# Kernel optimization log

Measured on AMD Instinct MI355X. Metric: run time of the kernel, lower is better.

## Reference

```python
import jax, jax.numpy as jnp
import numpy as np

B, N, D, C = 256, 200000, 128, 1000


def _l2_normalize(v, axis=-1, eps=1e-12):
    # matches torch F.normalize(p=2): v / max(||v||, eps)
    norm = jnp.sqrt(jnp.sum(v * v, axis=axis, keepdims=True))
    return v / jnp.maximum(norm, eps)


def setup_inputs() -> dict:
    key = jax.random.key(0)
    k1, k2, k3 = jax.random.split(key, 3)
    x = jax.random.normal(k1, (B, D), dtype=jnp.float32)
    index_embeddings = jax.random.normal(k2, (N, D), dtype=jnp.float32)
    class_labels = jax.random.randint(k3, (N,), 0, C, dtype=jnp.int32)
    return {
        "x": x,
        "index_embeddings": index_embeddings,
        "class_labels": class_labels,
        "num_classes": C,
    }


def reference(x, index_embeddings, class_labels, num_classes):
    # backbone output flattened -> embeddings [B, D]; L2-normalize (queries and index,
    # index normalization happens in add_index_data in the original module)
    emb = _l2_normalize(x)
    idx_emb = _l2_normalize(index_embeddings)
    # cosine similarities [B, N]
    similarities = jnp.einsum('bd,nd->bn', emb, idx_emb)
    # per-class max reduction (replaces Python loop over classes):
    # segment-max over the index dimension keyed by class_labels -> [B, num_classes]
    logits = jax.ops.segment_max(
        similarities.T, class_labels, num_segments=num_classes,
        indices_are_sorted=False,
    ).T
    return logits
```

## Files before the change

### kernel.cpp

```cpp
#include <hip/hip_runtime.h>
#include <hip/hip_bf16.h>
#include <stdint.h>

#define D_ 128
#define NB 64
#define NINF (-__builtin_inff())

typedef float f32x4 __attribute__((ext_vector_type(4)));
typedef short bf16x8 __attribute__((ext_vector_type(8)));

__device__ inline unsigned short f2bf(float f){
  unsigned x = __float_as_uint(f);
  return (unsigned short)((x + 0x7FFFu + ((x >> 16) & 1u)) >> 16);
}
__device__ inline unsigned packbf(float a, float b){
  return (unsigned)f2bf(a) | ((unsigned)f2bf(b) << 16);
}
__device__ inline unsigned fkey(float v){
  unsigned b = __float_as_uint(v);
  return (b & 0x80000000u) ? ~b : (b | 0x80000000u);
}

__global__ void k_prep(const float* __restrict__ emb, const float* __restrict__ x,
                       unsigned short* __restrict__ nrmlin, unsigned short* __restrict__ xn,
                       const int* __restrict__ lab, unsigned* __restrict__ hist,
                       int N, int B, int C, int PN, int XB, int HB){
  const int bid = blockIdx.x;
  const int t = threadIdx.x;
  if (bid < PN + XB){
    const float* src; unsigned short* dst; int nrows; int r0;
    if (bid < PN){ src = emb; dst = nrmlin; nrows = N; r0 = bid * 64; }
    else         { src = x;   dst = xn;     nrows = B; r0 = (bid - PN) * 64; }
    int r = r0 + (t >> 2);
    if (r >= nrows) return;
    int j = t & 3;
    const f32x4* s4 = reinterpret_cast<const f32x4*>(src + (size_t)r * D_ + j * 32);
    f32x4 v[8];
    #pragma unroll
    for (int i = 0; i < 8; i++) v[i] = s4[i];
    float ss = 0.f;
    #pragma unroll
    for (int i = 0; i < 8; i++) ss += v[i][0]*v[i][0] + v[i][1]*v[i][1] + v[i][2]*v[i][2] + v[i][3]*v[i][3];
    ss += __shfl_xor(ss, 1); ss += __shfl_xor(ss, 2);
    float sc = 1.0f / fmaxf(sqrtf(ss), 1e-12f);
    unsigned o[16];
    #pragma unroll
    for (int i = 0; i < 8; i++){
      o[i*2]   = packbf(v[i][0]*sc, v[i][1]*sc);
      o[i*2+1] = packbf(v[i][2]*sc, v[i][3]*sc);
    }
    uint4* d4 = reinterpret_cast<uint4*>(dst + (size_t)r * D_ + j * 32);
    #pragma unroll
    for (int i = 0; i < 4; i++) d4[i] = make_uint4(o[i*4], o[i*4+1], o[i*4+2], o[i*4+3]);
  } else {
    int hb = bid - PN - XB;
    __shared__ unsigned lh[1024];
    for (int c = t; c < 1024; c += 256) lh[c] = 0;
    __syncthreads();
    for (int i = hb * 256 + t; i < N; i += HB * 256) atomicAdd(&lh[lab[i]], 1u);
    __syncthreads();
    for (int c = t; c < C; c += 256){ unsigned v = lh[c]; if (v) atomicAdd(&hist[c], v); }
  }
}

__global__ void k_scan(const unsigned* __restrict__ hist, unsigned* __restrict__ cursor,
                       unsigned* __restrict__ cbase, int C){
  __shared__ unsigned s[1024];
  int t = threadIdx.x;
  unsigned v = (t < C) ? hist[t] : 0u;
  s[t] = v; __syncthreads();
  for (int off = 1; off < 1024; off <<= 1){
    unsigned u = (t >= off) ? s[t - off] : 0u;
    __syncthreads();
    s[t] += u;
    __syncthreads();
  }
  if (t < C){ unsigned e = s[t] - v; cursor[t] = e; cbase[t] = e; }
}

__global__ void k_scatter(const int* __restrict__ lab, unsigned* __restrict__ cursor,
                          int* __restrict__ perm, int* __restrict__ slab, int N){
  for (int i = blockIdx.x * 256 + threadIdx.x; i < N; i += gridDim.x * 256){
    int c = lab[i];
    unsigned pos = atomicAdd(&cursor[c], 1u);
    perm[pos] = i;
    slab[pos] = c;
  }
}

__global__ __launch_bounds__(256, 2) void k_gemm_cls(
    const unsigned short* __restrict__ nrmlin,
    const unsigned short* __restrict__ xn,
    const int* __restrict__ perm,
    const unsigned* __restrict__ cbase, const unsigned* __restrict__ hist,
    float* __restrict__ out, int N, int C){
  const int c = blockIdx.x;
  const int t = threadIdx.x, w = t >> 6, lane = t & 63, lr = lane & 15, lg = lane >> 4;
  const int nrows = (int)hist[c];
  if (nrows == 0){ out[(size_t)t * C + c] = NINF; return; }
  const int base = (int)cbase[c];
  const int last = base + nrows - 1;
  const int chunks = (nrows + NB - 1) >> 6;

  __shared__ __align__(16) unsigned short Ab[2][NB * D_];

  auto rid_load = [&](int ci, int (&r)[4]){
    int cc = ci < chunks ? ci : chunks - 1;
    #pragma unroll
    for (int i = 0; i < 4; i++){
      int gr = base + cc * NB + i * 16 + lr;
      if (gr > last) gr = last;
      r[i] = perm[gr];
    }
  };
  auto stage = [&](int bb, const int (&r)[4]){
    #pragma unroll
    for (int i = 0; i < 4; i++){
      const char* src = (const char*)nrmlin + (size_t)r[i] * 256 + ((w * 4 + lg) << 4);
      char* dst = (char*)(&Ab[bb][0]) + (w + i * 4) * 1024 + lane * 16;
      __builtin_amdgcn_global_load_lds(
          (const __attribute__((address_space(1))) unsigned int*)src,
          (__attribute__((address_space(3))) unsigned int*)dst, 16, 0, 0);
    }
  };

  int ridN[4];
  rid_load(0, ridN);
  stage(0, ridN);
  rid_load(1, ridN);

  bf16x8 bf[4][4];
  #pragma unroll
  for (int ni = 0; ni < 4; ni++)
    #pragma unroll
    for (int kk = 0; kk < 4; kk++)
      bf[ni][kk] = *reinterpret_cast<const bf16x8*>(
          xn + (size_t)(w * 64 + ni * 16 + lr) * D_ + kk * 32 + lg * 8);

  float M0 = NINF, M1 = NINF, M2 = NINF, M3 = NINF;

  for (int ci = 0; ci < chunks; ++ci){
    const int b = ci & 1;
    stage(b ^ 1, ridN);
    rid_load(ci + 2, ridN);
    __builtin_amdgcn_s_barrier();

    f32x4 acc[4][4];
    #pragma unroll
    for (int mi = 0; mi < 4; mi++)
      #pragma unroll
      for (int ni = 0; ni < 4; ni++)
        acc[mi][ni] = (f32x4){0.f, 0.f, 0.f, 0.f};

    #pragma unroll
    for (int mi = 0; mi < 4; mi++)
      #pragma unroll
      for (int kk = 0; kk < 4; kk++){
        bf16x8 af = *reinterpret_cast<const bf16x8*>(&Ab[b][(mi * 4 + kk) * 512 + lane * 8]);
        #pragma unroll
        for (int ni = 0; ni < 4; ni++)
          acc[mi][ni] = __builtin_amdgcn_mfma_f32_16x16x32_bf16(af, bf[ni][kk], acc[mi][ni], 0, 0, 0);
      }
    __builtin_amdgcn_s_barrier();

    #pragma unroll
    for (int mi = 0; mi < 4; mi++)
      #pragma unroll
      for (int rg = 0; rg < 4; rg++){
        M0 = fmaxf(M0, acc[mi][0][rg]);
        M1 = fmaxf(M1, acc[mi][1][rg]);
        M2 = fmaxf(M2, acc[mi][2][rg]);
        M3 = fmaxf(M3, acc[mi][3][rg]);
      }
  }
  asm volatile("s_waitcnt vmcnt(0)" ::: "memory");

  M0 = fmaxf(M0, __shfl_xor(M0, 16)); M0 = fmaxf(M0, __shfl_xor(M0, 32));
  M1 = fmaxf(M1, __shfl_xor(M1, 16)); M1 = fmaxf(M1, __shfl_xor(M1, 32));
  M2 = fmaxf(M2, __shfl_xor(M2, 16)); M2 = fmaxf(M2, __shfl_xor(M2, 32));
  M3 = fmaxf(M3, __shfl_xor(M3, 16)); M3 = fmaxf(M3, __shfl_xor(M3, 32));
  float mv = (lg < 2) ? ((lg == 0) ? M0 : M1) : ((lg == 2) ? M2 : M3);
  out[(size_t)t * C + c] = mv;
}

__global__ void k_init_out(unsigned* __restrict__ o, int n){
  int i = blockIdx.x * 256 + threadIdx.x;
  if (i < n) o[i] = 0x007FFFFFu;
}

struct __align__(16) GSm {
  unsigned short A[NB * 136];
  float sims[16 * 257];
  float scale[NB];
  int rowid[NB];
  int clab[NB];
};

__global__ __launch_bounds__(256, 2) void k_gemm_gather(
    const float* __restrict__ emb, const unsigned short* __restrict__ xn,
    const int* __restrict__ perm, const int* __restrict__ slab,
    unsigned* __restrict__ out_u, int N, int C){
  __shared__ GSm sm;
  const int t = threadIdx.x;
  const int base = blockIdx.x * NB;
  if (t < NB){
    int p = base + t; if (p > N - 1) p = N - 1;
    sm.rowid[t] = perm[p];
    sm.clab[t]  = slab[p];
  }
  __syncthreads();
  {
    int r = t >> 2, j = t & 3;
    const float4* src = reinterpret_cast<const float4*>(emb + (long)sm.rowid[r] * D_ + j * 32);
    float4 v[8];
    #pragma unroll
    for (int i = 0; i < 8; i++) v[i] = src[i];
    float ss = 0.f;
    #pragma unroll
    for (int i = 0; i < 8; i++) ss += v[i].x*v[i].x + v[i].y*v[i].y + v[i].z*v[i].z + v[i].w*v[i].w;
    ss += __shfl_xor(ss, 1); ss += __shfl_xor(ss, 2);
    sm.scale[r] = 1.0f / fmaxf(sqrtf(ss), 1e-12f);
    unsigned* dst = reinterpret_cast<unsigned*>(&sm.A[r * 136 + j * 32]);
    #pragma unroll
    for (int i = 0; i < 8; i++){
      dst[i * 2]     = packbf(v[i].x, v[i].y);
      dst[i * 2 + 1] = packbf(v[i].z, v[i].w);
    }
  }
  const int w = t >> 6, lane = t & 63;
  const int lr = lane & 15, lg = lane >> 4;
  bf16x8 bfr[4][4];
  #pragma unroll
  for (int ni = 0; ni < 4; ni++)
    #pragma unroll
    for (int kk = 0; kk < 4; kk++)
      bfr[ni][kk] = *reinterpret_cast<const bf16x8*>(
          xn + (size_t)(w * 64 + ni * 16 + lr) * D_ + kk * 32 + lg * 8);
  f32x4 acc[4][4];
  #pragma unroll
  for (int mi = 0; mi < 4; mi++)
    #pragma unroll
    for (int ni = 0; ni < 4; ni++)
      acc[mi][ni] = (f32x4){0.f, 0.f, 0.f, 0.f};
  __syncthreads();
  #pragma unroll
  for (int mi = 0; mi < 4; mi++)
    #pragma unroll
    for (int kk = 0; kk < 4; kk++){
      bf16x8 af = *reinterpret_cast<const bf16x8*>(&sm.A[(mi * 16 + lr) * 136 + kk * 32 + lg * 8]);
      #pragma unroll
      for (int ni = 0; ni < 4; ni++)
        acc[mi][ni] = __builtin_amdgcn_mfma_f32_16x16x32_bf16(af, bfr[ni][kk], acc[mi][ni], 0, 0, 0);
    }
  int cur = -1; float rm = 0.f;
  for (int mi = 0; mi < 4; mi++){
    __syncthreads();
    #pragma unroll
    for (int ni = 0; ni < 4; ni++)
      #pragma unroll
      for (int rg = 0; rg < 4; rg++){
        int r16 = lg * 4 + rg;
        sm.sims[r16 * 257 + w * 64 + ni * 16 + lr] = acc[mi][ni][rg] * sm.scale[mi * 16 + r16];
      }
    __syncthreads();
    #pragma unroll
    for (int r16 = 0; r16 < 16; r16++){
      int cc = sm.clab[mi * 16 + r16];
      float v = sm.sims[r16 * 257 + t];
      if (cc != cur){
        if (cur >= 0) atomicMax(&out_u[(size_t)t * C + cur], fkey(rm));
        cur = cc; rm = v;
      } else rm = fmaxf(rm, v);
    }
  }
  atomicMax(&out_u[(size_t)t * C + cur], fkey(rm));
}

__global__ void k_finalize(unsigned* __restrict__ o, int n){
  int i = blockIdx.x * 256 + threadIdx.x;
  if (i < n){
    unsigned k = o[i];
    o[i] = (k & 0x80000000u) ? (k & 0x7FFFFFFFu) : ~k;
  }
}

extern "C" void kernel_launch(void* const* d_in, const int* in_sizes, int n_in,
                              void* d_out, int out_size, void* d_ws, size_t ws_size,
                              hipStream_t stream){
  const float* x   = (const float*)d_in[0];
  const float* emb = (const float*)d_in[1];
  const int*   lab = (const int*)d_in[2];
  const int B = in_sizes[0] / D_;
  const int N = in_sizes[1] / D_;
  const int C = out_size / B;

  const int PNfull = (N + 63) / 64;
  const int XB = (B + 63) / 64;
  const int HB = 208;

  char* ws = (char*)d_ws;
  size_t off = 0;
  unsigned short* xn = (unsigned short*)(ws); off += ((size_t)B * D_ * 2 + 255) & ~(size_t)255;
  unsigned* hist   = (unsigned*)(ws + off); off += 4096;
  unsigned* cursor = (unsigned*)(ws + off); off += 4096;
  unsigned* cbase  = (unsigned*)(ws + off); off += 4096;
  size_t narr = ((size_t)N * 4 + 255) & ~(size_t)255;
  int* perm   = (int*)(ws + off); off += narr;
  int* slab   = (int*)(ws + off); off += narr;
  unsigned short* nrmlin = (unsigned short*)(ws + off);
  size_t need = off + (size_t)N * D_ * 2;
  const bool fast = (ws_size >= need);
  const int PN = fast ? PNfull : 0;

  hipMemsetAsync(hist, 0, 4096, stream);
  k_prep<<<PN + XB + HB, 256, 0, stream>>>(emb, x, nrmlin, xn, lab, hist,
                                           N, B, C, PN, XB, HB);
  k_scan<<<1, 1024, 0, stream>>>(hist, cursor, cbase, C);
  k_scatter<<<208, 256, 0, stream>>>(lab, cursor, perm, slab, N);
  if (fast){
    k_gemm_cls<<<C, 256, 0, stream>>>(nrmlin, xn, perm, cbase, hist,
                                      (float*)d_out, N, C);
  } else {
    const int IB = (B * C + 255) / 256;
    k_init_out<<<IB, 256, 0, stream>>>((unsigned*)d_out, B * C);
    k_gemm_gather<<<PNfull, 256, 0, stream>>>(emb, xn, perm, slab, (unsigned*)d_out, N, C);
    k_finalize<<<IB, 256, 0, stream>>>((unsigned*)d_out, B * C);
  }
}
```

Before: 243.1 us.

## Fuse all stages into one cooperative persistent kernel with grid syncs

Replaces the memset, prep, scan, scatter and per-class GEMM launches with a single cooperative kernel of 512 blocks. Stages are separated by grid.sync, and per-block histograms are reduced through a phist buffer instead of global atomics. The intent is to remove launch gaps and inter-kernel idle time. The cost is several grid-wide barriers and a fixed grid size that handles 1000 classes in about two waves, which may imbalance the GEMM phase. It falls back to the old multi-kernel path if the cooperative launch fails or the workspace is too small.

```diff
diff --git a/kernel.cpp b/kernel.cpp
--- a/kernel.cpp
+++ b/kernel.cpp
@@ -1,9 +1,13 @@
 #include <hip/hip_runtime.h>
 #include <hip/hip_bf16.h>
+#include <hip/hip_cooperative_groups.h>
 #include <stdint.h>
+
+namespace cg = cooperative_groups;
 
 #define D_ 128
 #define NB 64
+#define GB 512
 #define NINF (-__builtin_inff())
 
 typedef float f32x4 __attribute__((ext_vector_type(4)));
@@ -19,6 +23,187 @@
 __device__ inline unsigned fkey(float v){
   unsigned b = __float_as_uint(v);
   return (b & 0x80000000u) ? ~b : (b | 0x80000000u);
+}
+
+__device__ inline void norm_unit(const float* __restrict__ src, unsigned short* __restrict__ dst,
+                                 int r0, int t){
+  int r = r0 + (t >> 2), j = t & 3;
+  const f32x4* s4 = reinterpret_cast<const f32x4*>(src + (size_t)r * D_ + j * 32);
+  f32x4 v[8];
+  #pragma unroll
+  for (int i = 0; i < 8; i++) v[i] = s4[i];
+  float ss = 0.f;
+  #pragma unroll
+  for (int i = 0; i < 8; i++) ss += v[i][0]*v[i][0] + v[i][1]*v[i][1] + v[i][2]*v[i][2] + v[i][3]*v[i][3];
+  ss += __shfl_xor(ss, 1); ss += __shfl_xor(ss, 2);
+  float sc = 1.0f / fmaxf(sqrtf(ss), 1e-12f);
+  unsigned o[16];
+  #pragma unroll
+  for (int i = 0; i < 8; i++){
+    o[i*2]   = packbf(v[i][0]*sc, v[i][1]*sc);
+    o[i*2+1] = packbf(v[i][2]*sc, v[i][3]*sc);
+  }
+  uint4* d4 = reinterpret_cast<uint4*>(dst + (size_t)r * D_ + j * 32);
+  #pragma unroll
+  for (int i = 0; i < 4; i++) d4[i] = make_uint4(o[i*4], o[i*4+1], o[i*4+2], o[i*4+3]);
+}
+
+__global__ __launch_bounds__(256, 2) void k_all(
+    const float* __restrict__ emb, const float* __restrict__ x,
+    const int* __restrict__ lab,
+    unsigned short* __restrict__ nrmlin, unsigned short* __restrict__ xn,
+    unsigned* __restrict__ phist, unsigned* __restrict__ hist,
+    unsigned* __restrict__ cursor, unsigned* __restrict__ cbase,
+    int* __restrict__ perm, float* __restrict__ out,
+    int N, int B, int C){
+  cg::grid_group grid = cg::this_grid();
+  const int bid = blockIdx.x, t = threadIdx.x;
+  const int nblk = (int)gridDim.x;
+  const int w = t >> 6, lane = t & 63, lr = lane & 15, lg = lane >> 4;
+
+  __shared__ __align__(16) unsigned short Ab[2][NB * D_];
+  unsigned* lh = reinterpret_cast<unsigned*>(&Ab[0][0]);
+
+  for (int c = t; c < 1024; c += 256) lh[c] = 0;
+  __syncthreads();
+  const int PN = N >> 6;
+  const int XU = B >> 6;
+  for (int u = bid; u < PN + XU; u += nblk){
+    if (u < PN) norm_unit(emb, nrmlin, u * 64, t);
+    else        norm_unit(x,   xn,    (u - PN) * 64, t);
+  }
+  for (int i = bid * 256 + t; i < N; i += nblk * 256) atomicAdd(&lh[lab[i]], 1u);
+  __syncthreads();
+  for (int c = t; c < C; c += 256) phist[(size_t)bid * 1024 + c] = lh[c];
+  __threadfence();
+  grid.sync();
+
+  {
+    int gw = (bid << 2) + w;
+    for (int c = gw; c < C; c += nblk * 4){
+      int s = 0;
+      for (int p = lane; p < nblk; p += 64) s += (int)phist[(size_t)p * 1024 + c];
+      #pragma unroll
+      for (int m = 32; m >= 1; m >>= 1) s += __shfl_xor(s, m);
+      if (lane == 0) hist[c] = (unsigned)s;
+    }
+  }
+  __threadfence();
+  grid.sync();
+
+  if (bid == 0){
+    unsigned v[4]; unsigned s = 0;
+    #pragma unroll
+    for (int i = 0; i < 4; i++){ int c = t * 4 + i; v[i] = (c < C) ? hist[c] : 0u; s += v[i]; }
+    lh[t] = s; __syncthreads();
+    for (int off = 1; off < 256; off <<= 1){
+      unsigned u2 = (t >= off) ? lh[t - off] : 0u;
+      __syncthreads(); lh[t] += u2; __syncthreads();
+    }
+    unsigned run = lh[t] - s;
+    #pragma unroll
+    for (int i = 0; i < 4; i++){
+      int c = t * 4 + i;
+      if (c < C){ cursor[c] = run; cbase[c] = run; }
+      run += v[i];
+    }
+  }
+  __threadfence();
+  grid.sync();
+
+  for (int i = bid * 256 + t; i < N; i += nblk * 256){
+    int c = lab[i];
+    unsigned pos = atomicAdd(&cursor[c], 1u);
+    perm[pos] = i;
+  }
+  __threadfence();
+  grid.sync();
+
+  bf16x8 bf[4][4];
+  #pragma unroll
+  for (int ni = 0; ni < 4; ni++)
+    #pragma unroll
+    for (int kk = 0; kk < 4; kk++)
+      bf[ni][kk] = *reinterpret_cast<const bf16x8*>(
+          xn + (size_t)(w * 64 + ni * 16 + lr) * D_ + kk * 32 + lg * 8);
+
+  for (int c = bid; c < C; c += nblk){
+    const int nrows = (int)hist[c];
+    if (nrows == 0){ out[(size_t)t * C + c] = NINF; continue; }
+    const int base = (int)cbase[c];
+    const int last = base + nrows - 1;
+    const int chunks = (nrows + NB - 1) >> 6;
+
+    auto rid_load = [&](int ci, int (&r)[4]){
+      int cc = ci < chunks ? ci : chunks - 1;
+      #pragma unroll
+      for (int i = 0; i < 4; i++){
+        int gr = base + cc * NB + i * 16 + lr;
+        if (gr > last) gr = last;
+        r[i] = perm[gr];
+      }
+    };
+    auto stage = [&](int bb, const int (&r)[4]){
+      #pragma unroll
+      for (int i = 0; i < 4; i++){
+        const char* src = (const char*)nrmlin + (size_t)r[i] * 256 + ((w * 4 + lg) << 4);
+        char* dst = (char*)(&Ab[bb][0]) + (w + i * 4) * 1024 + lane * 16;
+        __builtin_amdgcn_global_load_lds(
+            (const __attribute__((address_space(1))) unsigned int*)src,
+            (__attribute__((address_space(3))) unsigned int*)dst, 16, 0, 0);
+      }
+    };
+
+    int ridN[4];
+    rid_load(0, ridN);
+    stage(0, ridN);
+    rid_load(1, ridN);
+
+    float M0 = NINF, M1 = NINF, M2 = NINF, M3 = NINF;
+
+    for (int ci = 0; ci < chunks; ++ci){
+      const int b = ci & 1;
+      stage(b ^ 1, ridN);
+      rid_load(ci + 2, ridN);
+      __builtin_amdgcn_s_barrier();
+
+      f32x4 acc[4][4];
+      #pragma unroll
+      for (int mi = 0; mi < 4; mi++)
+        #pragma unroll
+        for (int ni = 0; ni < 4; ni++)
+          acc[mi][ni] = (f32x4){0.f, 0.f, 0.f, 0.f};
+
+      #pragma unroll
+      for (int mi = 0; mi < 4; mi++)
+        #pragma unroll
+        for (int kk = 0; kk < 4; kk++){
+          bf16x8 af = *reinterpret_cast<const bf16x8*>(&Ab[b][(mi * 4 + kk) * 512 + lane * 8]);
+          #pragma unroll
+          for (int ni = 0; ni < 4; ni++)
+            acc[mi][ni] = __builtin_amdgcn_mfma_f32_16x16x32_bf16(af, bf[ni][kk], acc[mi][ni], 0, 0, 0);
+        }
+      __builtin_amdgcn_s_barrier();
+
+      #pragma unroll
+      for (int mi = 0; mi < 4; mi++)
+        #pragma unroll
+        for (int rg = 0; rg < 4; rg++){
+          M0 = fmaxf(M0, acc[mi][0][rg]);
+          M1 = fmaxf(M1, acc[mi][1][rg]);
+          M2 = fmaxf(M2, acc[mi][2][rg]);
+          M3 = fmaxf(M3, acc[mi][3][rg]);
+        }
+    }
+    asm volatile("s_waitcnt vmcnt(0)" ::: "memory");
+
+    M0 = fmaxf(M0, __shfl_xor(M0, 16)); M0 = fmaxf(M0, __shfl_xor(M0, 32));
+    M1 = fmaxf(M1, __shfl_xor(M1, 16)); M1 = fmaxf(M1, __shfl_xor(M1, 32));
+    M2 = fmaxf(M2, __shfl_xor(M2, 16)); M2 = fmaxf(M2, __shfl_xor(M2, 32));
+    M3 = fmaxf(M3, __shfl_xor(M3, 16)); M3 = fmaxf(M3, __shfl_xor(M3, 32));
+    float mv = (lg < 2) ? ((lg == 0) ? M0 : M1) : ((lg == 2) ? M2 : M3);
+    out[(size_t)t * C + c] = mv;
+  }
 }
 
 __global__ void k_prep(const float* __restrict__ emb, const float* __restrict__ x,
@@ -28,30 +213,8 @@
   const int bid = blockIdx.x;
   const int t = threadIdx.x;
   if (bid < PN + XB){
-    const float* src; unsigned short* dst; int nrows; int r0;
-    if (bid < PN){ src = emb; dst = nrmlin; nrows = N; r0 = bid * 64; }
-    else         { src = x;   dst = xn;     nrows = B; r0 = (bid - PN) * 64; }
-    int r = r0 + (t >> 2);
-    if (r >= nrows) return;
-    int j = t & 3;
-    const f32x4* s4 = reinterpret_cast<const f32x4*>(src + (size_t)r * D_ + j * 32);
-    f32x4 v[8];
-    #pragma unroll
-    for (int i = 0; i < 8; i++) v[i] = s4[i];
-    float ss = 0.f;
-    #pragma unroll
-    for (int i = 0; i < 8; i++) ss += v[i][0]*v[i][0] + v[i][1]*v[i][1] + v[i][2]*v[i][2] + v[i][3]*v[i][3];
-    ss += __shfl_xor(ss, 1); ss += __shfl_xor(ss, 2);
-    float sc = 1.0f / fmaxf(sqrtf(ss), 1e-12f);
-    unsigned o[16];
-    #pragma unroll
-    for (int i = 0; i < 8; i++){
-      o[i*2]   = packbf(v[i][0]*sc, v[i][1]*sc);
-      o[i*2+1] = packbf(v[i][2]*sc, v[i][3]*sc);
-    }
-    uint4* d4 = reinterpret_cast<uint4*>(dst + (size_t)r * D_ + j * 32);
-    #pragma unroll
-    for (int i = 0; i < 4; i++) d4[i] = make_uint4(o[i*4], o[i*4+1], o[i*4+2], o[i*4+3]);
+    if (bid < PN) norm_unit(emb, nrmlin, bid * 64, t);
+    else          norm_unit(x,   xn,    (bid - PN) * 64, t);
   } else {
     int hb = bid - PN - XB;
     __shared__ unsigned lh[1024];
@@ -304,26 +467,45 @@
   unsigned* hist   = (unsigned*)(ws + off); off += 4096;
   unsigned* cursor = (unsigned*)(ws + off); off += 4096;
   unsigned* cbase  = (unsigned*)(ws + off); off += 4096;
+  unsigned* phist  = (unsigned*)(ws + off); off += (size_t)GB * 1024 * 4;
   size_t narr = ((size_t)N * 4 + 255) & ~(size_t)255;
   int* perm   = (int*)(ws + off); off += narr;
   int* slab   = (int*)(ws + off); off += narr;
   unsigned short* nrmlin = (unsigned short*)(ws + off);
   size_t need = off + (size_t)N * D_ * 2;
   const bool fast = (ws_size >= need);
-  const int PN = fast ? PNfull : 0;
-
-  hipMemsetAsync(hist, 0, 4096, stream);
-  k_prep<<<PN + XB + HB, 256, 0, stream>>>(emb, x, nrmlin, xn, lab, hist,
-                                           N, B, C, PN, XB, HB);
-  k_scan<<<1, 1024, 0, stream>>>(hist, cursor, cbase, C);
-  k_scatter<<<208, 256, 0, stream>>>(lab, cursor, perm, slab, N);
-  if (fast){
-    k_gemm_cls<<<C, 256, 0, stream>>>(nrmlin, xn, perm, cbase, hist,
-                                      (float*)d_out, N, C);
-  } else {
-    const int IB = (B * C + 255) / 256;
-    k_init_out<<<IB, 256, 0, stream>>>((unsigned*)d_out, B * C);
-    k_gemm_gather<<<PNfull, 256, 0, stream>>>(emb, xn, perm, slab, (unsigned*)d_out, N, C);
-    k_finalize<<<IB, 256, 0, stream>>>((unsigned*)d_out, B * C);
-  }
-}
+
+  bool coop_ok = false;
+  if (fast && B == 256 && C <= 1000 && (N & 63) == 0 && (B & 63) == 0){
+    const float* a_emb = emb; const float* a_x = x; const int* a_lab = lab;
+    unsigned short* a_nrm = nrmlin; unsigned short* a_xn = xn;
+    unsigned* a_ph = phist; unsigned* a_h = hist; unsigned* a_cur = cursor; unsigned* a_cb = cbase;
+    int* a_perm = perm; float* a_out = (float*)d_out;
+    int a_N = N, a_B = B, a_C = C;
+    void* args[] = {(void*)&a_emb, (void*)&a_x, (void*)&a_lab, (void*)&a_nrm, (void*)&a_xn,
+                    (void*)&a_ph, (void*)&a_h, (void*)&a_cur, (void*)&a_cb,
+                    (void*)&a_perm, (void*)&a_out, (void*)&a_N, (void*)&a_B, (void*)&a_C};
+    hipError_t e = hipLaunchCooperativeKernel((void*)k_all, dim3(GB), dim3(256),
+                                              args, 0, stream);
+    coop_ok = (e == hipSuccess);
+    if (!coop_ok) (void)hipGetLastError();
+  }
+
+  if (!coop_ok){
+    hipMemsetAsync(hist, 0, 4096, stream);
+    const int PN = fast ? PNfull : 0;
+    k_prep<<<PN + XB + HB, 256, 0, stream>>>(emb, x, nrmlin, xn, lab, hist,
+                                             N, B, C, PN, XB, HB);
+    k_scan<<<1, 1024, 0, stream>>>(hist, cursor, cbase, C);
+    k_scatter<<<208, 256, 0, stream>>>(lab, cursor, perm, slab, N);
+    if (fast){
+      k_gemm_cls<<<C, 256, 0, stream>>>(nrmlin, xn, perm, cbase, hist,
+                                        (float*)d_out, N, C);
+    } else {
+      const int IB = (B * C + 255) / 256;
+      k_init_out<<<IB, 256, 0, stream>>>((unsigned*)d_out, B * C);
+      k_gemm_gather<<<PNfull, 256, 0, stream>>>(emb, xn, perm, slab, (unsigned*)d_out, N, C);
+      k_finalize<<<IB, 256, 0, stream>>>((unsigned*)d_out, B * C);
+    }
+  }
+}
```

Result: slower. 695.5 us (+186.1%).
